# Kernel optimization log

Measured on AMD Instinct MI355X. Metric: run time of the kernel, lower is better.

## Reference

```python
import jax, jax.numpy as jnp
import numpy as np

EMBED = 1024
HEADS = 16
HEAD_DIM = EMBED // HEADS
MLP_HIDDEN = 4096


def _layernorm(x, g, b, eps=1e-5):
    mu = jnp.mean(x, axis=-1, keepdims=True)
    var = jnp.mean(jnp.square(x - mu), axis=-1, keepdims=True)
    return (x - mu) * jax.lax.rsqrt(var + eps) * g + b


def setup_inputs() -> dict:
    key = jax.random.key(0)
    ks = jax.random.split(key, 8)
    s = 0.02
    return {
        "x": jax.random.normal(ks[0], (8, 1024, EMBED), dtype=jnp.float32),
        "qkv_w": jax.random.normal(ks[1], (EMBED, 3 * EMBED), dtype=jnp.float32) * s,
        "qkv_b": jnp.zeros((3 * EMBED,), jnp.float32),
        "proj_w": jax.random.normal(ks[2], (EMBED, EMBED), dtype=jnp.float32) * s,
        "proj_b": jnp.zeros((EMBED,), jnp.float32),
        "fc1_w": jax.random.normal(ks[3], (EMBED, MLP_HIDDEN), dtype=jnp.float32) * s,
        "fc1_b": jnp.zeros((MLP_HIDDEN,), jnp.float32),
        "fc2_w": jax.random.normal(ks[4], (MLP_HIDDEN, EMBED), dtype=jnp.float32) * s,
        "fc2_b": jnp.zeros((EMBED,), jnp.float32),
        "ln1_g": jnp.ones((EMBED,), jnp.float32),
        "ln1_b": jnp.zeros((EMBED,), jnp.float32),
        "ln2_g": jnp.ones((EMBED,), jnp.float32),
        "ln2_b": jnp.zeros((EMBED,), jnp.float32),
    }


def reference(x, qkv_w, qkv_b, proj_w, proj_b, fc1_w, fc1_b, fc2_w, fc2_b,
              ln1_g, ln1_b, ln2_g, ln2_b):
    B, N, C = x.shape
    scale = HEAD_DIM ** -0.5

    # --- MHSA on pre-norm input ---
    h = _layernorm(x, ln1_g, ln1_b)
    qkv = h @ qkv_w + qkv_b                      # [B,N,3C]
    qkv = qkv.reshape(B, N, 3, HEADS, HEAD_DIM)
    q, k, v = (qkv[:, :, i].transpose(0, 2, 1, 3) for i in range(3))  # [B,H,N,d]
    attn = jnp.einsum('bhqd,bhkd->bhqk', q, k) * scale
    attn = jax.nn.softmax(attn, axis=-1)
    o = jnp.einsum('bhqk,bhkd->bhqd', attn, v)   # [B,H,N,d]
    o = o.transpose(0, 2, 1, 3).reshape(B, N, C)
    x = x + (o @ proj_w + proj_b)

    # --- MLP ---
    h2 = _layernorm(x, ln2_g, ln2_b)
    h2 = jax.nn.gelu(h2 @ fc1_w + fc1_b, approximate=False)
    x = x + (h2 @ fc2_w + fc2_b)
    return x
```

## Files before the change

kernel.cpp:

```cpp
#include <hip/hip_runtime.h>
#include <hip/hip_bf16.h>

typedef __bf16 bf16x8 __attribute__((ext_vector_type(8)));
typedef float  f32x4  __attribute__((ext_vector_type(4)));
typedef unsigned short u16;

static __device__ __forceinline__ u16 f2bf(float f) {
  union { float f; unsigned u; } v; v.f = f;
  unsigned r = v.u + 0x7fffu + ((v.u >> 16) & 1u);
  return (u16)(r >> 16);
}

static __device__ __forceinline__ void gld16(const void* g, void* l) {
  __builtin_amdgcn_global_load_lds(
      (const __attribute__((address_space(1))) unsigned int*)g,
      (__attribute__((address_space(3))) unsigned int*)l, 16, 0, 0);
}

__global__ __launch_bounds__(256) void transpose_cast_k(
    const float* __restrict__ W, u16* __restrict__ Wt, int K, int N) {
  __shared__ float tile[32][33];
  const int t = threadIdx.x;
  const int n0 = blockIdx.x * 32, k0 = blockIdx.y * 32;
  const int r = t >> 3, c4 = (t & 7) * 4;
  const float4 v = *(const float4*)(W + (size_t)(k0 + r) * N + n0 + c4);
  tile[r][c4 + 0] = v.x; tile[r][c4 + 1] = v.y;
  tile[r][c4 + 2] = v.z; tile[r][c4 + 3] = v.w;
  __syncthreads();
  const int n = t >> 3, k4 = (t & 7) * 4;
  uint2 pk;
  pk.x = f2bf(tile[k4 + 0][n]) | ((unsigned)f2bf(tile[k4 + 1][n]) << 16);
  pk.y = f2bf(tile[k4 + 2][n]) | ((unsigned)f2bf(tile[k4 + 3][n]) << 16);
  *(uint2*)(Wt + (size_t)(n0 + n) * K + k0 + k4) = pk;
}

__global__ __launch_bounds__(256) void ln_cast_k(
    const float* __restrict__ x, const float* __restrict__ g,
    const float* __restrict__ b, u16* __restrict__ out) {
  __shared__ float red[2][4];
  const int t = threadIdx.x;
  const size_t row = blockIdx.x;
  const float4 v = *(const float4*)(x + row * 1024 + t * 4);
  float s = v.x + v.y + v.z + v.w;
  float ss = v.x * v.x + v.y * v.y + v.z * v.z + v.w * v.w;
  #pragma unroll
  for (int m = 1; m <= 32; m <<= 1) { s += __shfl_xor(s, m); ss += __shfl_xor(ss, m); }
  if ((t & 63) == 0) { red[0][t >> 6] = s; red[1][t >> 6] = ss; }
  __syncthreads();
  s  = red[0][0] + red[0][1] + red[0][2] + red[0][3];
  ss = red[1][0] + red[1][1] + red[1][2] + red[1][3];
  const float mu = s * (1.f / 1024.f);
  const float var = ss * (1.f / 1024.f) - mu * mu;
  const float rs = rsqrtf(var + 1e-5f);
  const float4 gv = *(const float4*)(g + t * 4);
  const float4 bv = *(const float4*)(b + t * 4);
  uint2 pk;
  pk.x = f2bf((v.x - mu) * rs * gv.x + bv.x) |
         ((unsigned)f2bf((v.y - mu) * rs * gv.y + bv.y) << 16);
  pk.y = f2bf((v.z - mu) * rs * gv.z + bv.z) |
         ((unsigned)f2bf((v.w - mu) * rs * gv.w + bv.w) << 16);
  *(uint2*)(out + row * 1024 + t * 4) = pk;
}

template <int EPI>
__global__ __launch_bounds__(256, 2) void gemm_bt_k(
    const u16* __restrict__ A, const u16* __restrict__ Bt,
    const float* __restrict__ bias, u16* __restrict__ Cb, float* __restrict__ Cf,
    const float* __restrict__ R, u16* __restrict__ vT, int M, int N, int K) {
  __shared__ u16 lA[128 * 64];
  __shared__ u16 lB[128 * 64];
  const int t = threadIdx.x;
  const int mt = M >> 7;
  const int tm = blockIdx.x % mt, tn = blockIdx.x / mt;
  const int lo = t & 15, hi = (t >> 4) & 3, wid = t >> 6;
  const int wm = wid >> 1, wn = wid & 1;
  const int srow = t >> 3, scol = (t & 7) * 8;
  const u16* ga = A + (size_t)(tm * 128 + srow) * K + scol;
  const u16* gb = Bt + (size_t)(tn * 128 + srow) * K + scol;
  f32x4 acc[4][4];
  #pragma unroll
  for (int i = 0; i < 4; ++i)
    #pragma unroll
    for (int j = 0; j < 4; ++j) acc[i][j] = (f32x4){0.f, 0.f, 0.f, 0.f};

  for (int k0 = 0; k0 < K; k0 += 64) {
    #pragma unroll
    for (int j = 0; j < 4; ++j) {
      gld16(ga + (size_t)32 * j * K + k0, &lA[(j * 256 + t) * 8]);
      gld16(gb + (size_t)32 * j * K + k0, &lB[(j * 256 + t) * 8]);
    }
    __syncthreads();
    #pragma unroll
    for (int kk = 0; kk < 2; ++kk) {
      bf16x8 af[4], bf[4];
      #pragma unroll
      for (int mi = 0; mi < 4; ++mi)
        af[mi] = *(const bf16x8*)&lA[(wm * 64 + mi * 16 + lo) * 64 + kk * 32 + hi * 8];
      #pragma unroll
      for (int ni = 0; ni < 4; ++ni)
        bf[ni] = *(const bf16x8*)&lB[(wn * 64 + ni * 16 + lo) * 64 + kk * 32 + hi * 8];
      #pragma unroll
      for (int mi = 0; mi < 4; ++mi)
        #pragma unroll
        for (int ni = 0; ni < 4; ++ni)
          acc[mi][ni] = __builtin_amdgcn_mfma_f32_16x16x32_bf16(af[mi], bf[ni], acc[mi][ni], 0, 0, 0);
    }
    __syncthreads();
  }

  #pragma unroll
  for (int ni = 0; ni < 4; ++ni) {
    const int col = tn * 128 + wn * 64 + ni * 16 + lo;
    const float bv = bias[col];
    #pragma unroll
    for (int mi = 0; mi < 4; ++mi) {
      const int row0 = tm * 128 + wm * 64 + mi * 16 + hi * 4;
      const f32x4 v = acc[mi][ni];
      float vals[4];
      #pragma unroll
      for (int r = 0; r < 4; ++r) {
        float val = v[r] + bv;
        if (EPI == 1) val = 0.5f * val * (1.f + erff(val * 0.70710678118f));
        vals[r] = val;
      }
      if (EPI == 2) {
        #pragma unroll
        for (int r = 0; r < 4; ++r) {
          const size_t idx = (size_t)(row0 + r) * N + col;
          Cf[idx] = vals[r] + R[idx];
        }
      } else {
        #pragma unroll
        for (int r = 0; r < 4; ++r)
          Cb[(size_t)(row0 + r) * N + col] = f2bf(vals[r]);
        if (EPI == 3 && col >= 2048) {
          const int bb = row0 >> 10, n = row0 & 1023;
          const int hh = (col - 2048) >> 6, d = col & 63;
          uint2 pk;
          pk.x = f2bf(vals[0]) | ((unsigned)f2bf(vals[1]) << 16);
          pk.y = f2bf(vals[2]) | ((unsigned)f2bf(vals[3]) << 16);
          *(uint2*)(vT + ((size_t)((bb * 16 + hh) * 64 + d) << 10) + n) = pk;
        }
      }
    }
  }
}

__global__ __launch_bounds__(256, 2) void attn_k(
    const u16* __restrict__ qkv, const u16* __restrict__ vT, u16* __restrict__ o) {
  __shared__ u16 lK[64 * 64];
  __shared__ u16 lV[64 * 64];
  __shared__ u16 lP[64 * 72];
  const int t = threadIdx.x;
  const int lo = t & 15, hi = (t >> 4) & 3, w = t >> 6;
  const int qt = blockIdx.x & 15, bh = blockIdx.x >> 4;
  const int b = bh >> 4, h = bh & 15;
  const int q0 = qt * 64;
  const u16* Qb = qkv + (size_t)b * 1024 * 3072 + h * 64;
  const u16* Kb = Qb + 1024;
  const u16* Vt = vT + (size_t)bh * 64 * 1024;

  bf16x8 qf[2];
  {
    const size_t q = q0 + w * 16 + lo;
    qf[0] = *(const bf16x8*)(Qb + q * 3072 + hi * 8);
    qf[1] = *(const bf16x8*)(Qb + q * 3072 + 32 + hi * 8);
  }
  f32x4 oacc[4];
  #pragma unroll
  for (int i = 0; i < 4; ++i) oacc[i] = (f32x4){0.f, 0.f, 0.f, 0.f};
  float m = -1e30f, lsum = 0.f;
  const int srow = t >> 3, scol = (t & 7) * 8;

  for (int kv0 = 0; kv0 < 1024; kv0 += 64) {
    __syncthreads();
    #pragma unroll
    for (int j = 0; j < 2; ++j) {
      const int row = j * 32 + srow;
      gld16(Kb + (size_t)(kv0 + row) * 3072 + scol, &lK[(j * 256 + t) * 8]);
      gld16(Vt + (size_t)row * 1024 + kv0 + scol, &lV[(j * 256 + t) * 8]);
    }
    __syncthreads();

    f32x4 s[4];
    #pragma unroll
    for (int i = 0; i < 4; ++i) s[i] = (f32x4){0.f, 0.f, 0.f, 0.f};
    #pragma unroll
    for (int kk = 0; kk < 2; ++kk) {
      #pragma unroll
      for (int mi = 0; mi < 4; ++mi) {
        const bf16x8 kf = *(const bf16x8*)&lK[(mi * 16 + lo) * 64 + kk * 32 + hi * 8];
        s[mi] = __builtin_amdgcn_mfma_f32_16x16x32_bf16(kf, qf[kk], s[mi], 0, 0, 0);
      }
    }
    float sv[16];
    float tmax = -1e30f;
    #pragma unroll
    for (int mi = 0; mi < 4; ++mi)
      #pragma unroll
      for (int r = 0; r < 4; ++r) {
        const float xx = s[mi][r] * 0.125f;
        sv[mi * 4 + r] = xx;
        tmax = fmaxf(tmax, xx);
      }
    tmax = fmaxf(tmax, __shfl_xor(tmax, 16));
    tmax = fmaxf(tmax, __shfl_xor(tmax, 32));
    const float mnew = fmaxf(m, tmax);
    const float alpha = __expf(m - mnew);
    m = mnew;
    float p[16], ts = 0.f;
    #pragma unroll
    for (int i = 0; i < 16; ++i) { p[i] = __expf(sv[i] - mnew); ts += p[i]; }
    ts += __shfl_xor(ts, 16);
    ts += __shfl_xor(ts, 32);
    lsum = lsum * alpha + ts;
    #pragma unroll
    for (int mi = 0; mi < 4; ++mi) {
      uint2 pk;
      pk.x = f2bf(p[mi * 4 + 0]) | ((unsigned)f2bf(p[mi * 4 + 1]) << 16);
      pk.y = f2bf(p[mi * 4 + 2]) | ((unsigned)f2bf(p[mi * 4 + 3]) << 16);
      *(uint2*)&lP[(w * 16 + lo) * 72 + mi * 16 + hi * 4] = pk;
    }
    asm volatile("s_waitcnt lgkmcnt(0)" ::: "memory");
    float ar[4];
    #pragma unroll
    for (int r = 0; r < 4; ++r) ar[r] = __shfl(alpha, hi * 4 + r);
    #pragma unroll
    for (int ni = 0; ni < 4; ++ni)
      #pragma unroll
      for (int r = 0; r < 4; ++r) oacc[ni][r] *= ar[r];
    #pragma unroll
    for (int kk = 0; kk < 2; ++kk) {
      const bf16x8 pf = *(const bf16x8*)&lP[(w * 16 + lo) * 72 + kk * 32 + hi * 8];
      #pragma unroll
      for (int ni = 0; ni < 4; ++ni) {
        const bf16x8 vf = *(const bf16x8*)&lV[(ni * 16 + lo) * 64 + kk * 32 + hi * 8];
        oacc[ni] = __builtin_amdgcn_mfma_f32_16x16x32_bf16(pf, vf, oacc[ni], 0, 0, 0);
      }
    }
  }
  float lr[4];
  #pragma unroll
  for (int r = 0; r < 4; ++r) lr[r] = 1.f / __shfl(lsum, hi * 4 + r);
  #pragma unroll
  for (int ni = 0; ni < 4; ++ni) {
    const int d = ni * 16 + lo;
    #pragma unroll
    for (int r = 0; r < 4; ++r) {
      const int n = q0 + w * 16 + hi * 4 + r;
      o[((size_t)(b * 1024 + n) * 16 + h) * 64 + d] = f2bf(oacc[ni][r] * lr[r]);
    }
  }
}

extern "C" void kernel_launch(void* const* d_in, const int* in_sizes, int n_in,
                              void* d_out, int out_size, void* d_ws, size_t ws_size,
                              hipStream_t stream) {
  const float* x      = (const float*)d_in[0];
  const float* qkv_w  = (const float*)d_in[1];
  const float* qkv_b  = (const float*)d_in[2];
  const float* proj_w = (const float*)d_in[3];
  const float* proj_b = (const float*)d_in[4];
  const float* fc1_w  = (const float*)d_in[5];
  const float* fc1_b  = (const float*)d_in[6];
  const float* fc2_w  = (const float*)d_in[7];
  const float* fc2_b  = (const float*)d_in[8];
  const float* ln1_g  = (const float*)d_in[9];
  const float* ln1_b  = (const float*)d_in[10];
  const float* ln2_g  = (const float*)d_in[11];
  const float* ln2_b  = (const float*)d_in[12];
  float* out = (float*)d_out;
  char* ws = (char*)d_ws;
  u16* wqkvT = (u16*)(ws);
  u16* wprojT = (u16*)(ws + 6291456);
  u16* wfc1T = (u16*)(ws + 8388608);
  u16* wfc2T = (u16*)(ws + 16777216);
  u16* hbuf  = (u16*)(ws + 25165824);
  u16* qkvo  = (u16*)(ws + 41943040);
  u16* vT    = (u16*)(ws + 92274688);
  u16* fc1o  = qkvo;

  transpose_cast_k<<<dim3(96, 32),  256, 0, stream>>>(qkv_w,  wqkvT, 1024, 3072);
  transpose_cast_k<<<dim3(32, 32),  256, 0, stream>>>(proj_w, wprojT, 1024, 1024);
  transpose_cast_k<<<dim3(128, 32), 256, 0, stream>>>(fc1_w,  wfc1T, 1024, 4096);
  transpose_cast_k<<<dim3(32, 128), 256, 0, stream>>>(fc2_w,  wfc2T, 4096, 1024);
  ln_cast_k<<<8192, 256, 0, stream>>>(x, ln1_g, ln1_b, hbuf);
  gemm_bt_k<3><<<64 * 24, 256, 0, stream>>>(hbuf, wqkvT, qkv_b, qkvo, nullptr, nullptr, vT, 8192, 3072, 1024);
  attn_k<<<2048, 256, 0, stream>>>(qkvo, vT, hbuf);
  gemm_bt_k<2><<<64 * 8, 256, 0, stream>>>(hbuf, wprojT, proj_b, nullptr, out, x, nullptr, 8192, 1024, 1024);
  ln_cast_k<<<8192, 256, 0, stream>>>(out, ln2_g, ln2_b, hbuf);
  gemm_bt_k<1><<<64 * 32, 256, 0, stream>>>(hbuf, wfc1T, fc1_b, fc1o, nullptr, nullptr, nullptr, 8192, 4096, 1024);
  gemm_bt_k<2><<<64 * 8, 256, 0, stream>>>(fc1o, wfc2T, fc2_b, nullptr, out, out, nullptr, 8192, 1024, 4096);
}
```

Measured before the change: 434.2 us.

## Replace GEMM with 256x256-tile 8-wave double-buffered pipelined kernel

```diff
diff --git a/kernel.cpp b/kernel.cpp
--- a/kernel.cpp
+++ b/kernel.cpp
@@ -16,6 +16,10 @@
       (const __attribute__((address_space(1))) unsigned int*)g,
       (__attribute__((address_space(3))) unsigned int*)l, 16, 0, 0);
 }
+
+#define SBAR() do { __builtin_amdgcn_sched_barrier(0); \
+                    __builtin_amdgcn_s_barrier(); \
+                    __builtin_amdgcn_sched_barrier(0); } while (0)
 
 __global__ __launch_bounds__(256) void transpose_cast_k(
     const float* __restrict__ W, u16* __restrict__ Wt, int K, int N) {
@@ -63,58 +67,123 @@
 }
 
 template <int EPI>
-__global__ __launch_bounds__(256, 2) void gemm_bt_k(
+__global__ __launch_bounds__(512, 2) void gemm8_k(
     const u16* __restrict__ A, const u16* __restrict__ Bt,
     const float* __restrict__ bias, u16* __restrict__ Cb, float* __restrict__ Cf,
     const float* __restrict__ R, u16* __restrict__ vT, int M, int N, int K) {
-  __shared__ u16 lA[128 * 64];
-  __shared__ u16 lB[128 * 64];
+  __shared__ u16 As[2][16384];
+  __shared__ u16 Bs[2][16384];
   const int t = threadIdx.x;
-  const int mt = M >> 7;
+  const int mt = M >> 8;
   const int tm = blockIdx.x % mt, tn = blockIdx.x / mt;
   const int lo = t & 15, hi = (t >> 4) & 3, wid = t >> 6;
-  const int wm = wid >> 1, wn = wid & 1;
-  const int srow = t >> 3, scol = (t & 7) * 8;
-  const u16* ga = A + (size_t)(tm * 128 + srow) * K + scol;
-  const u16* gb = Bt + (size_t)(tn * 128 + srow) * K + scol;
-  f32x4 acc[4][4];
-  #pragma unroll
-  for (int i = 0; i < 4; ++i)
+  const int wm = wid >> 2, wn = wid & 3;
+  const int NT = K >> 6;
+
+  const int srow = t >> 3;
+  const int sc = (t & 7) ^ (srow & 7);
+  const u16* gA = A  + (size_t)(tm * 256) * K;
+  const u16* gB = Bt + (size_t)(tn * 256) * K;
+  auto stA = [&](int dd, int c, int T) {
+    gld16(gA + (size_t)(c * 64 + srow) * K + (size_t)T * 64 + sc * 8,
+          &As[dd][c * 4096 + t * 8]);
+  };
+  auto stB = [&](int dd, int c, int T) {
+    gld16(gB + (size_t)(c * 64 + srow) * K + (size_t)T * 64 + sc * 8,
+          &Bs[dd][c * 4096 + t * 8]);
+  };
+
+  const int xr = lo & 7;
+  const int rowA = wm * 128 + lo;
+  const int rowB = wn * 64 + lo;
+#define RD_A(d, m, kk) (*(const bf16x8*)&As[d][(rowA + (m)*16)*64 + ((((kk)<<2)+hi)^xr)*8])
+#define RD_B(d, n, kk) (*(const bf16x8*)&Bs[d][(rowB + (n)*16)*64 + ((((kk)<<2)+hi)^xr)*8])
+#define MF(a, b, c) __builtin_amdgcn_mfma_f32_16x16x32_bf16(a, b, c, 0, 0, 0)
+
+  f32x4 acc[8][4];
+  #pragma unroll
+  for (int i = 0; i < 8; ++i)
     #pragma unroll
     for (int j = 0; j < 4; ++j) acc[i][j] = (f32x4){0.f, 0.f, 0.f, 0.f};
 
-  for (int k0 = 0; k0 < K; k0 += 64) {
-    #pragma unroll
-    for (int j = 0; j < 4; ++j) {
-      gld16(ga + (size_t)32 * j * K + k0, &lA[(j * 256 + t) * 8]);
-      gld16(gb + (size_t)32 * j * K + k0, &lB[(j * 256 + t) * 8]);
-    }
-    __syncthreads();
-    #pragma unroll
-    for (int kk = 0; kk < 2; ++kk) {
-      bf16x8 af[4], bf[4];
-      #pragma unroll
-      for (int mi = 0; mi < 4; ++mi)
-        af[mi] = *(const bf16x8*)&lA[(wm * 64 + mi * 16 + lo) * 64 + kk * 32 + hi * 8];
-      #pragma unroll
-      for (int ni = 0; ni < 4; ++ni)
-        bf[ni] = *(const bf16x8*)&lB[(wn * 64 + ni * 16 + lo) * 64 + kk * 32 + hi * 8];
-      #pragma unroll
-      for (int mi = 0; mi < 4; ++mi)
-        #pragma unroll
-        for (int ni = 0; ni < 4; ++ni)
-          acc[mi][ni] = __builtin_amdgcn_mfma_f32_16x16x32_bf16(af[mi], bf[ni], acc[mi][ni], 0, 0, 0);
-    }
-    __syncthreads();
+  stA(0, 0, 0); stA(0, 1, 0); stA(0, 2, 0); stA(0, 3, 0);
+  stB(0, 0, 0); stB(0, 1, 0); stB(0, 2, 0); stB(0, 3, 0);
+  stB(1, 0, 1); stB(1, 1, 1); stB(1, 2, 1); stB(1, 3, 1);
+  stA(1, 0, 1); stA(1, 2, 1);
+  asm volatile("s_waitcnt vmcnt(6)" ::: "memory");
+  SBAR();
+
+  for (int T = 0; T < NT; ++T) {
+    const int d = T & 1, dn = d ^ 1;
+    bf16x8 b00 = RD_B(d,0,0), b01 = RD_B(d,0,1), b10 = RD_B(d,1,0), b11 = RD_B(d,1,1);
+    bf16x8 b20 = RD_B(d,2,0), b21 = RD_B(d,2,1), b30 = RD_B(d,3,0), b31 = RD_B(d,3,1);
+    bf16x8 a00 = RD_A(d,0,0), a01 = RD_A(d,0,1), a10 = RD_A(d,1,0), a11 = RD_A(d,1,1);
+    if (T + 1 < NT) { stA(dn, 1, T + 1); stA(dn, 3, T + 1); }
+    SBAR();
+    __builtin_amdgcn_s_setprio(1);
+    acc[0][0]=MF(a00,b00,acc[0][0]); acc[0][0]=MF(a01,b01,acc[0][0]);
+    acc[0][1]=MF(a00,b10,acc[0][1]); acc[0][1]=MF(a01,b11,acc[0][1]);
+    acc[0][2]=MF(a00,b20,acc[0][2]); acc[0][2]=MF(a01,b21,acc[0][2]);
+    acc[0][3]=MF(a00,b30,acc[0][3]); acc[0][3]=MF(a01,b31,acc[0][3]);
+    acc[1][0]=MF(a10,b00,acc[1][0]); acc[1][0]=MF(a11,b01,acc[1][0]);
+    acc[1][1]=MF(a10,b10,acc[1][1]); acc[1][1]=MF(a11,b11,acc[1][1]);
+    acc[1][2]=MF(a10,b20,acc[1][2]); acc[1][2]=MF(a11,b21,acc[1][2]);
+    acc[1][3]=MF(a10,b30,acc[1][3]); acc[1][3]=MF(a11,b31,acc[1][3]);
+    __builtin_amdgcn_s_setprio(0);
+    SBAR();
+    a00 = RD_A(d,2,0); a01 = RD_A(d,2,1); a10 = RD_A(d,3,0); a11 = RD_A(d,3,1);
+    if (T + 2 < NT) { stB(d, 0, T + 2); stB(d, 1, T + 2); }
+    SBAR();
+    __builtin_amdgcn_s_setprio(1);
+    acc[2][0]=MF(a00,b00,acc[2][0]); acc[2][0]=MF(a01,b01,acc[2][0]);
+    acc[2][1]=MF(a00,b10,acc[2][1]); acc[2][1]=MF(a01,b11,acc[2][1]);
+    acc[2][2]=MF(a00,b20,acc[2][2]); acc[2][2]=MF(a01,b21,acc[2][2]);
+    acc[2][3]=MF(a00,b30,acc[2][3]); acc[2][3]=MF(a01,b31,acc[2][3]);
+    acc[3][0]=MF(a10,b00,acc[3][0]); acc[3][0]=MF(a11,b01,acc[3][0]);
+    acc[3][1]=MF(a10,b10,acc[3][1]); acc[3][1]=MF(a11,b11,acc[3][1]);
+    acc[3][2]=MF(a10,b20,acc[3][2]); acc[3][2]=MF(a11,b21,acc[3][2]);
+    acc[3][3]=MF(a10,b30,acc[3][3]); acc[3][3]=MF(a11,b31,acc[3][3]);
+    __builtin_amdgcn_s_setprio(0);
+    SBAR();
+    a00 = RD_A(d,4,0); a01 = RD_A(d,4,1); a10 = RD_A(d,5,0); a11 = RD_A(d,5,1);
+    if (T + 2 < NT) { stB(d, 2, T + 2); stB(d, 3, T + 2); }
+    SBAR();
+    __builtin_amdgcn_s_setprio(1);
+    acc[4][0]=MF(a00,b00,acc[4][0]); acc[4][0]=MF(a01,b01,acc[4][0]);
+    acc[4][1]=MF(a00,b10,acc[4][1]); acc[4][1]=MF(a01,b11,acc[4][1]);
+    acc[4][2]=MF(a00,b20,acc[4][2]); acc[4][2]=MF(a01,b21,acc[4][2]);
+    acc[4][3]=MF(a00,b30,acc[4][3]); acc[4][3]=MF(a01,b31,acc[4][3]);
+    acc[5][0]=MF(a10,b00,acc[5][0]); acc[5][0]=MF(a11,b01,acc[5][0]);
+    acc[5][1]=MF(a10,b10,acc[5][1]); acc[5][1]=MF(a11,b11,acc[5][1]);
+    acc[5][2]=MF(a10,b20,acc[5][2]); acc[5][2]=MF(a11,b21,acc[5][2]);
+    acc[5][3]=MF(a10,b30,acc[5][3]); acc[5][3]=MF(a11,b31,acc[5][3]);
+    __builtin_amdgcn_s_setprio(0);
+    SBAR();
+    a00 = RD_A(d,6,0); a01 = RD_A(d,6,1); a10 = RD_A(d,7,0); a11 = RD_A(d,7,1);
+    if (T + 2 < NT) { stA(d, 0, T + 2); stA(d, 2, T + 2); }
+    SBAR();
+    __builtin_amdgcn_s_setprio(1);
+    acc[6][0]=MF(a00,b00,acc[6][0]); acc[6][0]=MF(a01,b01,acc[6][0]);
+    acc[6][1]=MF(a00,b10,acc[6][1]); acc[6][1]=MF(a01,b11,acc[6][1]);
+    acc[6][2]=MF(a00,b20,acc[6][2]); acc[6][2]=MF(a01,b21,acc[6][2]);
+    acc[6][3]=MF(a00,b30,acc[6][3]); acc[6][3]=MF(a01,b31,acc[6][3]);
+    acc[7][0]=MF(a10,b00,acc[7][0]); acc[7][0]=MF(a11,b01,acc[7][0]);
+    acc[7][1]=MF(a10,b10,acc[7][1]); acc[7][1]=MF(a11,b11,acc[7][1]);
+    acc[7][2]=MF(a10,b20,acc[7][2]); acc[7][2]=MF(a11,b21,acc[7][2]);
+    acc[7][3]=MF(a10,b30,acc[7][3]); acc[7][3]=MF(a11,b31,acc[7][3]);
+    __builtin_amdgcn_s_setprio(0);
+    if (T < NT - 2)       { asm volatile("s_waitcnt vmcnt(6)" ::: "memory"); }
+    else if (T == NT - 2) { asm volatile("s_waitcnt vmcnt(0)" ::: "memory"); }
+    SBAR();
   }
 
   #pragma unroll
   for (int ni = 0; ni < 4; ++ni) {
-    const int col = tn * 128 + wn * 64 + ni * 16 + lo;
+    const int col = tn * 256 + wn * 64 + ni * 16 + lo;
     const float bv = bias[col];
     #pragma unroll
-    for (int mi = 0; mi < 4; ++mi) {
-      const int row0 = tm * 128 + wm * 64 + mi * 16 + hi * 4;
+    for (int mi = 0; mi < 8; ++mi) {
+      const int row0 = tm * 256 + wm * 128 + mi * 16 + hi * 4;
       const f32x4 v = acc[mi][ni];
       float vals[4];
       #pragma unroll
@@ -135,15 +204,18 @@
           Cb[(size_t)(row0 + r) * N + col] = f2bf(vals[r]);
         if (EPI == 3 && col >= 2048) {
           const int bb = row0 >> 10, n = row0 & 1023;
-          const int hh = (col - 2048) >> 6, d = col & 63;
+          const int hh = (col - 2048) >> 6, dd = col & 63;
           uint2 pk;
           pk.x = f2bf(vals[0]) | ((unsigned)f2bf(vals[1]) << 16);
           pk.y = f2bf(vals[2]) | ((unsigned)f2bf(vals[3]) << 16);
-          *(uint2*)(vT + ((size_t)((bb * 16 + hh) * 64 + d) << 10) + n) = pk;
+          *(uint2*)(vT + ((size_t)((bb * 16 + hh) * 64 + dd) << 10) + n) = pk;
         }
       }
     }
   }
+#undef RD_A
+#undef RD_B
+#undef MF
 }
 
 __global__ __launch_bounds__(256, 2) void attn_k(
@@ -285,10 +357,10 @@
   transpose_cast_k<<<dim3(128, 32), 256, 0, stream>>>(fc1_w,  wfc1T, 1024, 4096);
   transpose_cast_k<<<dim3(32, 128), 256, 0, stream>>>(fc2_w,  wfc2T, 4096, 1024);
   ln_cast_k<<<8192, 256, 0, stream>>>(x, ln1_g, ln1_b, hbuf);
-  gemm_bt_k<3><<<64 * 24, 256, 0, stream>>>(hbuf, wqkvT, qkv_b, qkvo, nullptr, nullptr, vT, 8192, 3072, 1024);
+  gemm8_k<3><<<32 * 12, 512, 0, stream>>>(hbuf, wqkvT, qkv_b, qkvo, nullptr, nullptr, vT, 8192, 3072, 1024);
   attn_k<<<2048, 256, 0, stream>>>(qkvo, vT, hbuf);
-  gemm_bt_k<2><<<64 * 8, 256, 0, stream>>>(hbuf, wprojT, proj_b, nullptr, out, x, nullptr, 8192, 1024, 1024);
+  gemm8_k<2><<<32 * 4, 512, 0, stream>>>(hbuf, wprojT, proj_b, nullptr, out, x, nullptr, 8192, 1024, 1024);
   ln_cast_k<<<8192, 256, 0, stream>>>(out, ln2_g, ln2_b, hbuf);
-  gemm_bt_k<1><<<64 * 32, 256, 0, stream>>>(hbuf, wfc1T, fc1_b, fc1o, nullptr, nullptr, nullptr, 8192, 4096, 1024);
-  gemm_bt_k<2><<<64 * 8, 256, 0, stream>>>(fc1o, wfc2T, fc2_b, nullptr, out, out, nullptr, 8192, 1024, 4096);
-}
+  gemm8_k<1><<<32 * 16, 512, 0, stream>>>(hbuf, wfc1T, fc1_b, fc1o, nullptr, nullptr, nullptr, 8192, 4096, 1024);
+  gemm8_k<2><<<32 * 4, 512, 0, stream>>>(fc1o, wfc2T, fc2_b, nullptr, out, out, nullptr, 8192, 1024, 4096);
+}
```

Result: slower. 461.3 us (+6.2%).
